# Performance work log

Hardware: AMD Instinct MI355X
Metric: run time of the kernel (lower is better)

Reference implementation:

```python
import jax, jax.numpy as jnp
import numpy as np

N_NODES = 50000
N_EDGES = 1600000
IN_DIM = 128
OUT_DIM = 128


def setup_inputs() -> dict:
    key = jax.random.key(0)
    k_h, k_e, k_wm, k_wu, k_bu = jax.random.split(key, 5)
    h = jax.random.normal(k_h, (N_NODES, IN_DIM), dtype=jnp.float32)
    edge_index = jax.random.randint(k_e, (2, N_EDGES), 0, N_NODES, dtype=jnp.int64)
    # nn.Linear weights: W_msg [out, in] no bias; W_upd [out, in+out] with bias
    s1 = 1.0 / np.sqrt(IN_DIM)
    s2 = 1.0 / np.sqrt(IN_DIM + OUT_DIM)
    W_msg = jax.random.uniform(k_wm, (OUT_DIM, IN_DIM), jnp.float32, -s1, s1)
    W_upd = jax.random.uniform(k_wu, (OUT_DIM, IN_DIM + OUT_DIM), jnp.float32, -s2, s2)
    b_upd = jax.random.uniform(k_bu, (OUT_DIM,), jnp.float32, -s2, s2)
    return {"h": h, "edge_index": edge_index, "W_msg": W_msg, "W_upd": W_upd, "b_upd": b_upd}


def reference(h, edge_index, W_msg, W_upd, b_upd):
    src, dst = edge_index[0], edge_index[1]
    # gather -> linear: messages [E, out_dim]
    messages = jnp.einsum("ei,oi->eo", h[src], W_msg)
    # scatter-add aggregation into [N, out_dim]
    agg = jax.ops.segment_sum(messages, dst, num_segments=h.shape[0])
    # concat -> linear -> relu
    hu = jnp.concatenate([h, agg], axis=1)
    return jax.nn.relu(jnp.einsum("ni,oi->no", hu, W_upd) + b_upd)
```

## Files before the change

### kernel.cpp

```cpp
#include <hip/hip_runtime.h>
#include <hip/hip_bf16.h>

#define NN   50000
#define NE   1600000
#define D    128
#define NBK  3125
#define CAP2 768
#define EPB  8192
#define FILLB 196
#define ASTR 136
#define PREP_BLKS 3125
#define WPREP_BLKS 32

typedef __attribute__((ext_vector_type(8))) short short8;
typedef __attribute__((ext_vector_type(4))) float f32x4;

__device__ __forceinline__ unsigned short f2b(float x) {
  unsigned u = __float_as_uint(x);
  u += 0x7fffu + ((u >> 16) & 1u);
  return (unsigned short)(u >> 16);
}
__device__ __forceinline__ float b2f(unsigned v) {
  return __uint_as_float(v << 16);
}
__device__ __forceinline__ float b2fh(unsigned v) {
  return __uint_as_float(v & 0xffff0000u);
}

__global__ __launch_bounds__(512) void fused_k(const float* __restrict__ h,
                                               unsigned short* __restrict__ hb,
                                               int* __restrict__ gcur,
                                               const float* __restrict__ Wm,
                                               const float* __restrict__ Wu,
                                               unsigned short* __restrict__ W1b,
                                               unsigned short* __restrict__ Wcb,
                                               const int* __restrict__ ei,
                                               unsigned* __restrict__ ebuf) {
  __shared__ int cnt[NBK];
  __shared__ int off[NBK];
  __shared__ int nz;
  const int blk = blockIdx.x, tid = threadIdx.x;

  if (blk >= FILLB) {
    if (blk < FILLB + PREP_BLKS) {
      int i = (blk - FILLB) * 512 + tid;
      float4 x = ((const float4*)h)[i];
      ushort4 o;
      o.x = f2b(x.x); o.y = f2b(x.y); o.z = f2b(x.z); o.w = f2b(x.w);
      ((ushort4*)hb)[i] = o;
    } else {
      int t2 = (blk - FILLB - PREP_BLKS) * 512 + tid;
      if (t2 < 16384) {
        int o = t2 >> 7, j = t2 & 127;
        W1b[t2] = f2b(Wu[o * 256 + j]);
        float acc = 0.f;
#pragma unroll 4
        for (int k = 0; k < 128; ++k)
          acc += Wu[o * 256 + 128 + k] * Wm[k * 128 + j];
        Wcb[t2] = f2b(acc);
      }
    }
    return;
  }

  if (tid == 0) nz = 0;
  for (int t = tid; t < NBK; t += 512) cnt[t] = 0;
  __syncthreads();
  if (tid < 256) {
    int idx = 1 + 2 * (tid * (NE / 256));
    if (ei[idx] != 0) atomicOr(&nz, 1);
  }
  __syncthreads();
  const int f = (nz == 0);

  const int e0 = blk * EPB + tid * 16;
  unsigned p[16]; int lr[16];
  if (e0 + 16 <= NE) {
    if (f) {
      const int4* ps = (const int4*)(ei + 2 * (size_t)e0);
      const int4* pd = (const int4*)(ei + 2 * (size_t)NE + 2 * (size_t)e0);
#pragma unroll
      for (int j2 = 0; j2 < 8; ++j2) {
        int4 a = ps[j2];
        int4 c = pd[j2];
        p[2 * j2]     = (unsigned)a.x | ((unsigned)c.x << 16);
        p[2 * j2 + 1] = (unsigned)a.z | ((unsigned)c.z << 16);
      }
    } else {
      const int4* ps = (const int4*)(ei + e0);
      const int4* pd = (const int4*)(ei + (size_t)NE + e0);
#pragma unroll
      for (int j2 = 0; j2 < 4; ++j2) {
        int4 a = ps[j2];
        int4 c = pd[j2];
        p[4 * j2 + 0] = (unsigned)a.x | ((unsigned)c.x << 16);
        p[4 * j2 + 1] = (unsigned)a.y | ((unsigned)c.y << 16);
        p[4 * j2 + 2] = (unsigned)a.z | ((unsigned)c.z << 16);
        p[4 * j2 + 3] = (unsigned)a.w | ((unsigned)c.w << 16);
      }
    }
#pragma unroll
    for (int j = 0; j < 16; ++j)
      lr[j] = atomicAdd(&cnt[p[j] >> 20], 1);
  } else {
#pragma unroll 1
    for (int j = 0; j < 16; ++j) {
      int e = e0 + j;
      p[j] = 0xffffffffu;
      if (e < NE) {
        int src = f ? ei[2 * (size_t)e] : ei[e];
        int dst = f ? ei[2 * ((size_t)NE + e)] : ei[NE + e];
        p[j] = (unsigned)src | ((unsigned)dst << 16);
        lr[j] = atomicAdd(&cnt[p[j] >> 20], 1);
      }
    }
  }
  __syncthreads();
  for (int t = tid; t < NBK; t += 512)
    off[t] = cnt[t] ? atomicAdd(&gcur[t], cnt[t]) : 0;
  __syncthreads();
#pragma unroll
  for (int j = 0; j < 16; ++j) {
    if (p[j] != 0xffffffffu) {
      int bk = (int)(p[j] >> 20);
      int idx = off[bk] + lr[j];
      if (idx < CAP2) ebuf[(size_t)bk * CAP2 + idx] = p[j] & 0xfffffu;
    }
  }
}

__global__ __launch_bounds__(256, 8) void sortagg_k(const unsigned* __restrict__ ebuf,
                                                    const int* __restrict__ gcur,
                                                    const unsigned short* __restrict__ hb,
                                                    const unsigned short* __restrict__ W1b,
                                                    const unsigned short* __restrict__ Wcb,
                                                    const float* __restrict__ bias,
                                                    float* __restrict__ out) {
  __shared__ unsigned short srt[CAP2];
  __shared__ __align__(16) unsigned short aggL[16 * ASTR];
  __shared__ int cnt[16];
  __shared__ int ofs[17];
  __shared__ int cur[16];
  const int b = blockIdx.x, tid = threadIdx.x;
  const int lane = tid & 63, wv = tid >> 6;
  if (tid < 16) cnt[tid] = 0;
  __syncthreads();
  const int count = min(gcur[b], CAP2);
  const unsigned* eb = ebuf + (size_t)b * CAP2;
  for (int e = tid; e < count; e += 256)
    atomicAdd(&cnt[eb[e] >> 16], 1);
  __syncthreads();
  if (wv == 0) {
    int v = (lane < 16) ? cnt[lane] : 0;
    int s = v;
#pragma unroll
    for (int d = 1; d < 16; d <<= 1) {
      int t = __shfl_up(s, d, 64);
      if (lane >= d) s += t;
    }
    if (lane < 16) {
      ofs[lane] = s - v;
      cur[lane] = s - v;
    }
    if (lane == 0) ofs[16] = count;
  }
  __syncthreads();
  for (int e = tid; e < count; e += 256) {
    unsigned p = eb[e];
    int slot = atomicAdd(&cur[p >> 16], 1);
    srt[slot] = (unsigned short)(p & 0xffffu);
  }
  __syncthreads();

  const int q = lane >> 4;
  const int r = lane & 15;
  const unsigned short* hbl = hb + r * 8;
#pragma unroll 1
  for (int k = 0; k < 4; ++k) {
    const int n = wv * 4 + k;
    const int beg = ofs[n], end = ofs[n + 1];
    float a0=0.f,a1=0.f,a2=0.f,a3=0.f,a4=0.f,a5=0.f,a6=0.f,a7=0.f;
    int e = beg;
    for (; e + 32 <= end; e += 32) {
      uint4 vv[8];
#pragma unroll
      for (int j = 0; j < 8; ++j)
        vv[j] = *(const uint4*)(hbl + (size_t)srt[e + 4 * j + q] * D);
#pragma unroll
      for (int j = 0; j < 8; ++j) {
        a0 += b2f(vv[j].x & 0xffffu); a1 += b2fh(vv[j].x);
        a2 += b2f(vv[j].y & 0xffffu); a3 += b2fh(vv[j].y);
        a4 += b2f(vv[j].z & 0xffffu); a5 += b2fh(vv[j].z);
        a6 += b2f(vv[j].w & 0xffffu); a7 += b2fh(vv[j].w);
      }
    }
    if (e < end) {
      uint4 vv[8];
#pragma unroll
      for (int j = 0; j < 8; ++j) {
        const int edge = e + 4 * j + q;
        const int ce = min(edge, end - 1);
        vv[j] = *(const uint4*)(hbl + (size_t)srt[ce] * D);
      }
#pragma unroll
      for (int j = 0; j < 8; ++j) {
        const int edge = e + 4 * j + q;
        if (edge >= end) { vv[j].x = 0u; vv[j].y = 0u; vv[j].z = 0u; vv[j].w = 0u; }
        a0 += b2f(vv[j].x & 0xffffu); a1 += b2fh(vv[j].x);
        a2 += b2f(vv[j].y & 0xffffu); a3 += b2fh(vv[j].y);
        a4 += b2f(vv[j].z & 0xffffu); a5 += b2fh(vv[j].z);
        a6 += b2f(vv[j].w & 0xffffu); a7 += b2fh(vv[j].w);
      }
    }
    a0 += __shfl_xor(a0, 16, 64); a0 += __shfl_xor(a0, 32, 64);
    a1 += __shfl_xor(a1, 16, 64); a1 += __shfl_xor(a1, 32, 64);
    a2 += __shfl_xor(a2, 16, 64); a2 += __shfl_xor(a2, 32, 64);
    a3 += __shfl_xor(a3, 16, 64); a3 += __shfl_xor(a3, 32, 64);
    a4 += __shfl_xor(a4, 16, 64); a4 += __shfl_xor(a4, 32, 64);
    a5 += __shfl_xor(a5, 16, 64); a5 += __shfl_xor(a5, 32, 64);
    a6 += __shfl_xor(a6, 16, 64); a6 += __shfl_xor(a6, 32, 64);
    a7 += __shfl_xor(a7, 16, 64); a7 += __shfl_xor(a7, 32, 64);
    if (lane < 16) {
      uint4 o;
      o.x = (unsigned)f2b(a0) | ((unsigned)f2b(a1) << 16);
      o.y = (unsigned)f2b(a2) | ((unsigned)f2b(a3) << 16);
      o.z = (unsigned)f2b(a4) | ((unsigned)f2b(a5) << 16);
      o.w = (unsigned)f2b(a6) | ((unsigned)f2b(a7) << 16);
      *(uint4*)(aggL + n * ASTR + r * 8) = o;
    }
  }
  __syncthreads();

  const int rr = lane & 15, g = lane >> 4;
  const int t0 = wv * 2;
  const int nodeA = b * 16 + rr;

  f32x4 accm[2];
#pragma unroll
  for (int t = 0; t < 2; ++t) accm[t] = (f32x4){0.f, 0.f, 0.f, 0.f};

#pragma unroll
  for (int c = 0; c < 8; ++c) {
    const int k0 = (c & 3) * 32 + g * 8;
    short8 a;
    if (c < 4) {
      a = *(const short8*)(hb + (size_t)nodeA * D + k0);
    } else {
      a = *(const short8*)(aggL + rr * ASTR + k0);
    }
    const unsigned short* W = (c < 4) ? W1b : Wcb;
#pragma unroll
    for (int tt = 0; tt < 2; ++tt) {
      short8 bfr = *(const short8*)(W + (size_t)((t0 + tt) * 16 + rr) * D + k0);
      accm[tt] = __builtin_amdgcn_mfma_f32_16x16x32_bf16(a, bfr, accm[tt], 0, 0, 0);
    }
  }

#pragma unroll
  for (int tt = 0; tt < 2; ++tt) {
    const int col = (t0 + tt) * 16 + rr;
    const float bv = bias[col];
#pragma unroll
    for (int j = 0; j < 4; ++j) {
      const int orow = b * 16 + g * 4 + j;
      float vv = accm[tt][j] + bv;
      out[(size_t)orow * D + col] = vv > 0.f ? vv : 0.f;
    }
  }
}

extern "C" void kernel_launch(void* const* d_in, const int* in_sizes, int n_in,
                              void* d_out, int out_size, void* d_ws, size_t ws_size,
                              hipStream_t stream) {
  const float* h  = (const float*)d_in[0];
  const int*   ei = (const int*)d_in[1];
  const float* Wm = (const float*)d_in[2];
  const float* Wu = (const float*)d_in[3];
  const float* bu = (const float*)d_in[4];
  float* out = (float*)d_out;

  char* ws = (char*)d_ws;
  unsigned short* hb   = (unsigned short*)(ws);
  unsigned*       ebuf = (unsigned*)(ws + 12800000);
  int*            gcur = (int*)(ws + 22400000);
  unsigned short* W1b  = (unsigned short*)(ws + 22412512);
  unsigned short* Wcb  = (unsigned short*)(ws + 22445280);

  hipMemsetAsync(gcur, 0, NBK * sizeof(int), stream);
  fused_k<<<FILLB + PREP_BLKS + WPREP_BLKS, 512, 0, stream>>>(
      h, hb, gcur, Wm, Wu, W1b, Wcb, ei, ebuf);
  sortagg_k<<<NBK, 256, 0, stream>>>(ebuf, gcur, hb, W1b, Wcb, bu, out);
}
```

Baseline: 110.8 us.

## Use 1024-thread blocks with one wave per node for gather aggregation

The aggregation kernel grows from 256 to 1024 threads per block, so each of the 16 waves handles one destination node. Each lane now loads one 4-byte bf16 pair per edge across 16 edges, instead of quarter-waves loading 16-byte chunks and reducing across lanes with shuffles. The MFMA update stage is restricted to 8 waves, each computing one 16-column tile. The aim is more memory-level parallelism per block and no cross-lane reductions, at the cost of narrower per-lane loads, more threads per block and idle waves during the MFMA phase.

New measurement: 126.8 us. +14.5%, slower.

```diff
diff --git a/kernel.cpp b/kernel.cpp
--- a/kernel.cpp
+++ b/kernel.cpp
@@ -129,13 +129,13 @@
   }
 }
 
-__global__ __launch_bounds__(256, 8) void sortagg_k(const unsigned* __restrict__ ebuf,
-                                                    const int* __restrict__ gcur,
-                                                    const unsigned short* __restrict__ hb,
-                                                    const unsigned short* __restrict__ W1b,
-                                                    const unsigned short* __restrict__ Wcb,
-                                                    const float* __restrict__ bias,
-                                                    float* __restrict__ out) {
+__global__ __launch_bounds__(1024, 8) void sortagg_k(const unsigned* __restrict__ ebuf,
+                                                     const int* __restrict__ gcur,
+                                                     const unsigned short* __restrict__ hb,
+                                                     const unsigned short* __restrict__ W1b,
+                                                     const unsigned short* __restrict__ Wcb,
+                                                     const float* __restrict__ bias,
+                                                     float* __restrict__ out) {
   __shared__ unsigned short srt[CAP2];
   __shared__ __align__(16) unsigned short aggL[16 * ASTR];
   __shared__ int cnt[16];
@@ -147,7 +147,7 @@
   __syncthreads();
   const int count = min(gcur[b], CAP2);
   const unsigned* eb = ebuf + (size_t)b * CAP2;
-  for (int e = tid; e < count; e += 256)
+  for (int e = tid; e < count; e += 1024)
     atomicAdd(&cnt[eb[e] >> 16], 1);
   __syncthreads();
   if (wv == 0) {
@@ -165,105 +165,70 @@
     if (lane == 0) ofs[16] = count;
   }
   __syncthreads();
-  for (int e = tid; e < count; e += 256) {
+  for (int e = tid; e < count; e += 1024) {
     unsigned p = eb[e];
     int slot = atomicAdd(&cur[p >> 16], 1);
     srt[slot] = (unsigned short)(p & 0xffffu);
   }
   __syncthreads();
 
-  const int q = lane >> 4;
-  const int r = lane & 15;
-  const unsigned short* hbl = hb + r * 8;
-#pragma unroll 1
-  for (int k = 0; k < 4; ++k) {
-    const int n = wv * 4 + k;
-    const int beg = ofs[n], end = ofs[n + 1];
-    float a0=0.f,a1=0.f,a2=0.f,a3=0.f,a4=0.f,a5=0.f,a6=0.f,a7=0.f;
+  {
+    const int beg = ofs[wv], end = ofs[wv + 1];
+    const unsigned short* hbl = hb + 2 * lane;
+    float ax0 = 0.f, ay0 = 0.f, ax1 = 0.f, ay1 = 0.f;
     int e = beg;
-    for (; e + 32 <= end; e += 32) {
-      uint4 vv[8];
-#pragma unroll
-      for (int j = 0; j < 8; ++j)
-        vv[j] = *(const uint4*)(hbl + (size_t)srt[e + 4 * j + q] * D);
-#pragma unroll
-      for (int j = 0; j < 8; ++j) {
-        a0 += b2f(vv[j].x & 0xffffu); a1 += b2fh(vv[j].x);
-        a2 += b2f(vv[j].y & 0xffffu); a3 += b2fh(vv[j].y);
-        a4 += b2f(vv[j].z & 0xffffu); a5 += b2fh(vv[j].z);
-        a6 += b2f(vv[j].w & 0xffffu); a7 += b2fh(vv[j].w);
+    for (; e + 16 <= end; e += 16) {
+      unsigned u[16];
+#pragma unroll
+      for (int j = 0; j < 16; ++j)
+        u[j] = *(const unsigned*)(hbl + (size_t)srt[e + j] * D);
+#pragma unroll
+      for (int j = 0; j < 16; j += 2) {
+        ax0 += b2f(u[j] & 0xffffu);     ay0 += b2fh(u[j]);
+        ax1 += b2f(u[j + 1] & 0xffffu); ay1 += b2fh(u[j + 1]);
       }
     }
     if (e < end) {
-      uint4 vv[8];
-#pragma unroll
-      for (int j = 0; j < 8; ++j) {
-        const int edge = e + 4 * j + q;
-        const int ce = min(edge, end - 1);
-        vv[j] = *(const uint4*)(hbl + (size_t)srt[ce] * D);
-      }
-#pragma unroll
-      for (int j = 0; j < 8; ++j) {
-        const int edge = e + 4 * j + q;
-        if (edge >= end) { vv[j].x = 0u; vv[j].y = 0u; vv[j].z = 0u; vv[j].w = 0u; }
-        a0 += b2f(vv[j].x & 0xffffu); a1 += b2fh(vv[j].x);
-        a2 += b2f(vv[j].y & 0xffffu); a3 += b2fh(vv[j].y);
-        a4 += b2f(vv[j].z & 0xffffu); a5 += b2fh(vv[j].z);
-        a6 += b2f(vv[j].w & 0xffffu); a7 += b2fh(vv[j].w);
-      }
-    }
-    a0 += __shfl_xor(a0, 16, 64); a0 += __shfl_xor(a0, 32, 64);
-    a1 += __shfl_xor(a1, 16, 64); a1 += __shfl_xor(a1, 32, 64);
-    a2 += __shfl_xor(a2, 16, 64); a2 += __shfl_xor(a2, 32, 64);
-    a3 += __shfl_xor(a3, 16, 64); a3 += __shfl_xor(a3, 32, 64);
-    a4 += __shfl_xor(a4, 16, 64); a4 += __shfl_xor(a4, 32, 64);
-    a5 += __shfl_xor(a5, 16, 64); a5 += __shfl_xor(a5, 32, 64);
-    a6 += __shfl_xor(a6, 16, 64); a6 += __shfl_xor(a6, 32, 64);
-    a7 += __shfl_xor(a7, 16, 64); a7 += __shfl_xor(a7, 32, 64);
-    if (lane < 16) {
-      uint4 o;
-      o.x = (unsigned)f2b(a0) | ((unsigned)f2b(a1) << 16);
-      o.y = (unsigned)f2b(a2) | ((unsigned)f2b(a3) << 16);
-      o.z = (unsigned)f2b(a4) | ((unsigned)f2b(a5) << 16);
-      o.w = (unsigned)f2b(a6) | ((unsigned)f2b(a7) << 16);
-      *(uint4*)(aggL + n * ASTR + r * 8) = o;
-    }
-  }
-  __syncthreads();
-
-  const int rr = lane & 15, g = lane >> 4;
-  const int t0 = wv * 2;
-  const int nodeA = b * 16 + rr;
-
-  f32x4 accm[2];
-#pragma unroll
-  for (int t = 0; t < 2; ++t) accm[t] = (f32x4){0.f, 0.f, 0.f, 0.f};
-
-#pragma unroll
-  for (int c = 0; c < 8; ++c) {
-    const int k0 = (c & 3) * 32 + g * 8;
-    short8 a;
-    if (c < 4) {
-      a = *(const short8*)(hb + (size_t)nodeA * D + k0);
-    } else {
-      a = *(const short8*)(aggL + rr * ASTR + k0);
-    }
-    const unsigned short* W = (c < 4) ? W1b : Wcb;
-#pragma unroll
-    for (int tt = 0; tt < 2; ++tt) {
-      short8 bfr = *(const short8*)(W + (size_t)((t0 + tt) * 16 + rr) * D + k0);
-      accm[tt] = __builtin_amdgcn_mfma_f32_16x16x32_bf16(a, bfr, accm[tt], 0, 0, 0);
-    }
-  }
-
-#pragma unroll
-  for (int tt = 0; tt < 2; ++tt) {
-    const int col = (t0 + tt) * 16 + rr;
+      unsigned u[16];
+#pragma unroll
+      for (int j = 0; j < 16; ++j) {
+        const int ce = min(e + j, end - 1);
+        u[j] = *(const unsigned*)(hbl + (size_t)srt[ce] * D);
+      }
+#pragma unroll
+      for (int j = 0; j < 16; ++j) {
+        if (e + j < end) { ax0 += b2f(u[j] & 0xffffu); ay0 += b2fh(u[j]); }
+      }
+    }
+    const float ax = ax0 + ax1, ay = ay0 + ay1;
+    *(unsigned*)(aggL + wv * ASTR + 2 * lane) =
+        (unsigned)f2b(ax) | ((unsigned)f2b(ay) << 16);
+  }
+  __syncthreads();
+
+  if (wv < 8) {
+    const int rr = lane & 15, g = lane >> 4;
+    const int nodeA = b * 16 + rr;
+    f32x4 accm = (f32x4){0.f, 0.f, 0.f, 0.f};
+#pragma unroll
+    for (int c = 0; c < 8; ++c) {
+      const int k0 = (c & 3) * 32 + g * 8;
+      short8 a;
+      if (c < 4) {
+        a = *(const short8*)(hb + (size_t)nodeA * D + k0);
+      } else {
+        a = *(const short8*)(aggL + rr * ASTR + k0);
+      }
+      const unsigned short* W = (c < 4) ? W1b : Wcb;
+      short8 bfr = *(const short8*)(W + (size_t)(wv * 16 + rr) * D + k0);
+      accm = __builtin_amdgcn_mfma_f32_16x16x32_bf16(a, bfr, accm, 0, 0, 0);
+    }
+    const int col = wv * 16 + rr;
     const float bv = bias[col];
 #pragma unroll
     for (int j = 0; j < 4; ++j) {
       const int orow = b * 16 + g * 4 + j;
-      float vv = accm[tt][j] + bv;
+      float vv = accm[j] + bv;
       out[(size_t)orow * D + col] = vv > 0.f ? vv : 0.f;
     }
   }
@@ -289,5 +254,5 @@
   hipMemsetAsync(gcur, 0, NBK * sizeof(int), stream);
   fused_k<<<FILLB + PREP_BLKS + WPREP_BLKS, 512, 0, stream>>>(
       h, hb, gcur, Wm, Wu, W1b, Wcb, ei, ebuf);
-  sortagg_k<<<NBK, 256, 0, stream>>>(ebuf, gcur, hb, W1b, Wcb, bu, out);
-}
+  sortagg_k<<<NBK, 1024, 0, stream>>>(ebuf, gcur, hb, W1b, Wcb, bu, out);
+}
```
